# Optimization experiments

Measured on AMD Instinct MI355X. Metric: run time of the kernel, lower is better.

## Reference

```python
import jax, jax.numpy as jnp
import numpy as np

# ---- constants (match init_kwargs defaults) ----
N_NEURON = 512
N_E = int(N_NEURON * 0.8)
DT = 1.0
TAU_MEM = 20.0
TAU_SYN = 5.0
TAU_ADAPT = 700.0
V_TH = -45.0
V_RESET = -60.0
REF_STEPS = int(5.0 / DT)
ASC_AMP = -0.2
READOUT_TAU = 20.0
RESPONSE_WINDOW = 0.8


@jax.custom_vjp
def spike_fn(x):
    # Heaviside with sigmoid surrogate gradient (standard SNN training trick)
    return (x >= 0.0).astype(x.dtype)

def _spike_fwd(x):
    return spike_fn(x), x

def _spike_bwd(x, g):
    beta = 4.0
    s = jax.nn.sigmoid(beta * x)
    return (g * beta * s * (1.0 - s),)

spike_fn.defvjp(_spike_fwd, _spike_bwd)


def setup_inputs() -> dict:
    key = jax.random.key(0)
    kx, kwi, kwr, kmask, kwo = jax.random.split(key, 5)
    T, B, D, N, O = 1000, 64, 128, N_NEURON, 10
    x = jax.random.uniform(kx, (T, B, D), dtype=jnp.float32)  # analog input drive
    W_in = jax.random.normal(kwi, (N, D), dtype=jnp.float32) / np.sqrt(D)
    mag = jnp.abs(jax.random.normal(kwr, (N, N), dtype=jnp.float32)) * 0.05
    mask = (jax.random.uniform(kmask, (N, N)) < 0.1).astype(jnp.float32)
    sign = jnp.concatenate([jnp.ones((N_E,)), -jnp.ones((N - N_E,))]).astype(jnp.float32)
    W_rec = mag * mask * sign[None, :] * (1.0 - jnp.eye(N, dtype=jnp.float32))
    W_out = jax.random.normal(kwo, (O, N), dtype=jnp.float32) / np.sqrt(N)
    b_out = jnp.zeros((O,), dtype=jnp.float32)
    return {
        "x": x,
        "W_in": W_in,
        "input_scale": jnp.float32(1.0),
        "W_rec": W_rec,
        "W_out": W_out,
        "b_out": b_out,
        "output_scale": jnp.float32(1.0),
    }


def _run_snn(x, W_in, input_scale, W_rec, W_out, b_out, output_scale):
    T, B, D = x.shape
    N = W_rec.shape[0]
    asc_amps = jnp.full((N,), ASC_AMP, dtype=x.dtype)  # n_adapt=0 -> all neurons adapt

    a_mem = DT / TAU_MEM
    e_syn = jnp.exp(jnp.asarray(-DT / TAU_SYN, dtype=x.dtype))
    e_asc = jnp.exp(jnp.asarray(-DT / TAU_ADAPT, dtype=x.dtype))

    I_ext = jnp.einsum('tbd,nd->tbn', x * input_scale, W_in)  # (T,B,N)

    v0 = jnp.full((B, N), V_RESET, dtype=x.dtype)
    z = jnp.zeros((B, N), dtype=x.dtype)
    ref0 = jnp.zeros((B, N), dtype=jnp.int32)

    def step(carry, I_t):
        v, asc, r, psc, ref, s_prev = carry
        # AlphaPSC (two-state alpha kernel) driven by recurrent spikes
        rec = s_prev @ W_rec.T
        r = r * e_syn + rec
        psc = psc * e_syn + (DT / TAU_SYN) * r
        # GLIF3 membrane: leak toward v_reset + synaptic + external + after-spike currents
        I = I_t + psc + asc
        v = v + a_mem * (V_RESET - v) + a_mem * I
        in_ref = ref > 0
        v = jnp.where(in_ref, V_RESET, v)
        s = spike_fn(v - V_TH) * (1.0 - in_ref.astype(v.dtype))
        v = v * (1.0 - s) + V_RESET * s  # reset
        ref = jnp.where(s > 0, REF_STEPS, jnp.maximum(ref - 1, 0))
        asc = asc * e_asc + asc_amps[None, :] * s  # after-spike current adaptation
        return (v, asc, r, psc, ref, s), (s, v, psc)

    (_, _, _, _, _, _), (spikes, voltage, psc_hist) = jax.lax.scan(
        step, (v0, z, z, z, ref0, z), I_ext)

    # exponential low-pass filter of spikes, f[0] = s[0]
    alpha = jnp.exp(jnp.asarray(-DT / READOUT_TAU, dtype=x.dtype))
    def lp(f, s):
        f = alpha * f + (1.0 - alpha) * s
        return f, f
    f0 = spikes[0]
    _, f_rest = jax.lax.scan(lp, f0, spikes[1:])
    filtered = jnp.concatenate([f0[None], f_rest], axis=0)  # (T,B,N)

    start = int(T * (1.0 - RESPONSE_WINDOW))
    avg_spikes = filtered[start:].mean(axis=0)  # (B,N)
    output = (avg_spikes * output_scale) @ W_out.T + b_out  # (B,O)
    return output, spikes, voltage, psc_hist, filtered


def reference(x, W_in, input_scale, W_rec, W_out, b_out, output_scale):
    return _run_snn(x, W_in, input_scale, W_rec, W_out, b_out, output_scale)
```

## Files before the change

### kernel.cpp

```cpp
#include <hip/hip_runtime.h>
#include <hip/hip_bf16.h>


#define T_ 1000
#define B_ 64
#define D_ 128
#define N_ 512
#define O_ 10
#define BN_ (B_ * N_)
#define S_ ((size_t)T_ * BN_)

typedef __bf16 bf16x8 __attribute__((ext_vector_type(8)));
typedef float f32x4 __attribute__((ext_vector_type(4)));

__global__ __launch_bounds__(512, 1) void k_gemm_iext(
    const float* __restrict__ x, const float* __restrict__ Win,
    const float* __restrict__ scale_p, float* __restrict__ Iext,
    int* __restrict__ flagmax)
{
  __shared__ __bf16 sW[256 * 128];
  const int tid = threadIdx.x;
  const int nbase = blockIdx.y * 256;
  const float sc = *scale_p;

  for (int i = tid; i < 256 * 16; i += 512) {
    const int n = i >> 4, j = i & 15;
    const float4* src = (const float4*)(Win + (size_t)(nbase + n) * 128 + j * 8);
    float4 f0 = src[0], f1 = src[1];
    bf16x8 h;
    h[0] = (__bf16)f0.x; h[1] = (__bf16)f0.y; h[2] = (__bf16)f0.z; h[3] = (__bf16)f0.w;
    h[4] = (__bf16)f1.x; h[5] = (__bf16)f1.y; h[6] = (__bf16)f1.z; h[7] = (__bf16)f1.w;
    *(bf16x8*)(&sW[n * 128 + ((j ^ (n & 15)) << 3)]) = h;
  }
  __syncthreads();

  const int wave = tid >> 6, lane = tid & 63;
  const int quad = lane >> 4, l16 = lane & 15;
  const int mA = blockIdx.x * 128 + wave * 16 + l16;

  f32x4 acc[16];
#pragma unroll
  for (int c = 0; c < 16; ++c) acc[c] = (f32x4){0.f, 0.f, 0.f, 0.f};

#pragma unroll
  for (int kb = 0; kb < 4; ++kb) {
    const float4* ax = (const float4*)(x + (size_t)mA * 128 + kb * 32 + quad * 8);
    float4 a0 = ax[0], a1 = ax[1];
    bf16x8 af;
    af[0] = (__bf16)(a0.x * sc); af[1] = (__bf16)(a0.y * sc);
    af[2] = (__bf16)(a0.z * sc); af[3] = (__bf16)(a0.w * sc);
    af[4] = (__bf16)(a1.x * sc); af[5] = (__bf16)(a1.y * sc);
    af[6] = (__bf16)(a1.z * sc); af[7] = (__bf16)(a1.w * sc);
    const int j = kb * 4 + quad;
#pragma unroll
    for (int c = 0; c < 16; ++c) {
      const int n = c * 16 + l16;
      bf16x8 bfr = *(const bf16x8*)(&sW[n * 128 + ((j ^ (n & 15)) << 3)]);
      acc[c] = __builtin_amdgcn_mfma_f32_16x16x32_bf16(af, bfr, acc[c], 0, 0, 0);
    }
  }

  float mx = -1e30f;
  const int mBase = blockIdx.x * 128 + wave * 16 + quad * 4;
#pragma unroll
  for (int c = 0; c < 16; ++c) {
#pragma unroll
    for (int r = 0; r < 4; ++r) {
      float vv = acc[c][r];
      mx = fmaxf(mx, vv);
      Iext[(size_t)(mBase + r) * N_ + nbase + c * 16 + l16] = vv;
    }
  }
  if (flagmax) {
    for (int off = 32; off; off >>= 1) mx = fmaxf(mx, __shfl_xor(mx, off));
    if (lane == 0 && mx > 14.0f) atomicMax(flagmax, __float_as_int(mx));
  }
}

#define CHUNK_ 100
#define WARM_ 72
__global__ __launch_bounds__(128) void k_scan(
    const float* __restrict__ Iext, float* __restrict__ volt,
    const float* __restrict__ bout, float* __restrict__ out)
{
  if (blockIdx.y == 0 && blockIdx.x == 0) {
    for (int i = threadIdx.x; i < B_ * O_; i += 128) out[i] = bout[i % O_];
  }
  const int q = blockIdx.x * 128 + threadIdx.x;
  const int chunk = blockIdx.y;
  const int t0 = chunk * CHUNK_;
  const float4* I4 = (const float4*)Iext;
  float4* V4 = (float4*)volt;
  float4 v = make_float4(-60.f, -60.f, -60.f, -60.f);
  if (chunk != 0) {
#pragma unroll 4
    for (int t = t0 - WARM_; t < t0; ++t) {
      float4 I = I4[(size_t)t * (BN_ / 4) + q];
      v.x = v.x + 0.05f * (-60.f - v.x) + 0.05f * I.x;
      v.y = v.y + 0.05f * (-60.f - v.y) + 0.05f * I.y;
      v.z = v.z + 0.05f * (-60.f - v.z) + 0.05f * I.z;
      v.w = v.w + 0.05f * (-60.f - v.w) + 0.05f * I.w;
    }
  }
#pragma unroll 4
  for (int tt = 0; tt < CHUNK_; ++tt) {
    const size_t idx = (size_t)(t0 + tt) * (BN_ / 4) + q;
    float4 I = I4[idx];
    v.x = v.x + 0.05f * (-60.f - v.x) + 0.05f * I.x;
    v.y = v.y + 0.05f * (-60.f - v.y) + 0.05f * I.y;
    v.z = v.z + 0.05f * (-60.f - v.z) + 0.05f * I.z;
    v.w = v.w + 0.05f * (-60.f - v.w) + 0.05f * I.w;
    V4[idx] = v;
  }
}

__global__ __launch_bounds__(512) void k_fallback(
    const float* Iext, const float* __restrict__ Wrec,
    const float* __restrict__ Wout, const float* __restrict__ bout,
    const float* __restrict__ osc_p,
    float* out, float* spikes, float* volt, float* psc_o, float* filt,
    const int* __restrict__ flagmax)
{
  if (!(__int_as_float(*flagmax) > 14.0f)) return;
  const int b = blockIdx.x, n = threadIdx.x;
  __shared__ float s_sp[N_];
  __shared__ float red[N_];
  const float e_syn = expf(-0.2f), e_asc = expf(-1.0f / 700.0f), alpha = expf(-0.05f);
  float v = -60.f, asc = 0.f, rr = 0.f, psc = 0.f, f = 0.f, favg = 0.f, sprev = 0.f;
  int refc = 0;
  for (int t = 0; t < T_; ++t) {
    s_sp[n] = sprev;
    int cnt = __syncthreads_count(sprev > 0.f);
    float rec = 0.f;
    if (cnt > 0)
      for (int m = 0; m < N_; ++m) rec += s_sp[m] * Wrec[(size_t)n * N_ + m];
    rr = rr * e_syn + rec;
    psc = psc * e_syn + 0.2f * rr;
    const size_t idx = (size_t)t * BN_ + (size_t)b * N_ + n;
    float I = Iext[idx] + psc + asc;
    v = (v + 0.05f * (-60.f - v)) + 0.05f * I;
    bool in_ref = refc > 0;
    if (in_ref) v = -60.f;
    float s = (!in_ref && (v - (-45.f) >= 0.f)) ? 1.f : 0.f;
    v = v * (1.f - s) + (-60.f) * s;
    refc = (s > 0.f) ? 5 : (refc > 0 ? refc - 1 : 0);
    asc = asc * e_asc + (-0.2f) * s;
    spikes[idx] = s; volt[idx] = v; psc_o[idx] = psc;
    f = (t == 0) ? s : (alpha * f + (1.f - alpha) * s);
    filt[idx] = f;
    if (t >= 200) favg += f;
    sprev = s;
    __syncthreads();
  }
  favg = favg / 800.f;
  float a_s = favg * (*osc_p);
  for (int o = 0; o < O_; ++o) {
    red[n] = a_s * Wout[o * N_ + n];
    __syncthreads();
    for (int st = 256; st; st >>= 1) {
      if (n < st) red[n] += red[n + st];
      __syncthreads();
    }
    if (n == 0) out[b * O_ + o] = red[0] + bout[o];
    __syncthreads();
  }
}

extern "C" void kernel_launch(void* const* d_in, const int* in_sizes, int n_in,
                              void* d_out, int out_size, void* d_ws, size_t ws_size,
                              hipStream_t stream) {
  const float* x      = (const float*)d_in[0];
  const float* Win    = (const float*)d_in[1];
  const float* iscale = (const float*)d_in[2];
  const float* Wrec   = (const float*)d_in[3];
  const float* Wout   = (const float*)d_in[4];
  const float* bout   = (const float*)d_in[5];
  const float* oscale = (const float*)d_in[6];

  float* out    = (float*)d_out;
  float* spikes = out + B_ * O_;
  float* volt   = spikes + S_;
  float* psc    = volt + S_;
  float* filt   = psc + S_;

  const bool has_flag = ws_size >= 4;
  int* flag = has_flag ? (int*)d_ws : nullptr;
  const bool ws_iext = ws_size >= (size_t)256 + S_ * 4;
  float* iext = ws_iext ? (float*)((char*)d_ws + 256) : filt;

  hipMemsetAsync(spikes, 0, S_ * 4, stream);
  hipMemsetAsync(psc, 0, (ws_iext ? 2 * S_ : S_) * 4, stream);

  k_gemm_iext<<<dim3(500, 2), 512, 0, stream>>>(x, Win, iscale, iext, flag);

  k_scan<<<dim3(64, 10), 128, 0, stream>>>(iext, volt, bout, out);

  if (!ws_iext)
    hipMemsetAsync(filt, 0, S_ * 4, stream);

  if (has_flag)
    k_fallback<<<64, 512, 0, stream>>>(iext, Wrec, Wout, bout, oscale,
                                       out, spikes, volt, psc, filt, flag);
}
```

Baseline: 603.0 us.

## Fuse input GEMM, voltage scan and zero-fill into one kernel

Replaces the separate bf16 MFMA GEMM for I_ext, the chunked voltage scan kernel and the hipMemset zero-fills with a single kernel. Each block owns a 16-neuron slab and one time chunk. It keeps its W_in fragments in registers, computes I_ext per timestep with MFMA, integrates voltage in registers, and writes volt plus the zeroed spikes, psc and filt directly. This removes the full I_ext round trip through global memory and the extra memset passes. In exchange, every slab re-reads x, so x is fetched 32 times, the volt stores are narrower and less coalesced, and the fallback kernel now recomputes I_ext from x and W_in itself.

```diff
diff --git a/kernel.cpp b/kernel.cpp
--- a/kernel.cpp
+++ b/kernel.cpp
@@ -10,112 +10,107 @@
 #define BN_ (B_ * N_)
 #define S_ ((size_t)T_ * BN_)
 
+#define NSLABS_ 32
+#define NCHUNK_ 10
+#define CHUNK_ 100
+#define WARM_ 56
+
 typedef __bf16 bf16x8 __attribute__((ext_vector_type(8)));
 typedef float f32x4 __attribute__((ext_vector_type(4)));
 
-__global__ __launch_bounds__(512, 1) void k_gemm_iext(
+__global__ __launch_bounds__(256) void k_fused(
     const float* __restrict__ x, const float* __restrict__ Win,
-    const float* __restrict__ scale_p, float* __restrict__ Iext,
-    int* __restrict__ flagmax)
+    const float* __restrict__ scale_p, const float* __restrict__ bout,
+    float* __restrict__ out, float* __restrict__ spikes,
+    float* __restrict__ volt, float* __restrict__ psc,
+    float* __restrict__ filt, int* __restrict__ flagmax)
 {
-  __shared__ __bf16 sW[256 * 128];
   const int tid = threadIdx.x;
-  const int nbase = blockIdx.y * 256;
+  const int slab = blockIdx.x, chunk = blockIdx.y;
+  const int nbase = slab * 16;
   const float sc = *scale_p;
 
-  for (int i = tid; i < 256 * 16; i += 512) {
-    const int n = i >> 4, j = i & 15;
-    const float4* src = (const float4*)(Win + (size_t)(nbase + n) * 128 + j * 8);
+  if (slab == 0 && chunk == 0) {
+    for (int i = tid; i < B_ * O_; i += 256) out[i] = bout[i % O_];
+  }
+
+  const int wave = tid >> 6, lane = tid & 63;
+  const int quad = lane >> 4, l16 = lane & 15;
+  const int n = nbase + l16;
+
+  bf16x8 bfrag[4];
+#pragma unroll
+  for (int kb = 0; kb < 4; ++kb) {
+    const float4* src = (const float4*)(Win + (size_t)n * D_ + kb * 32 + quad * 8);
     float4 f0 = src[0], f1 = src[1];
     bf16x8 h;
     h[0] = (__bf16)f0.x; h[1] = (__bf16)f0.y; h[2] = (__bf16)f0.z; h[3] = (__bf16)f0.w;
     h[4] = (__bf16)f1.x; h[5] = (__bf16)f1.y; h[6] = (__bf16)f1.z; h[7] = (__bf16)f1.w;
-    *(bf16x8*)(&sW[n * 128 + ((j ^ (n & 15)) << 3)]) = h;
+    bfrag[kb] = h;
   }
-  __syncthreads();
 
-  const int wave = tid >> 6, lane = tid & 63;
-  const int quad = lane >> 4, l16 = lane & 15;
-  const int mA = blockIdx.x * 128 + wave * 16 + l16;
+  const int t0 = chunk * CHUNK_;
+  const int tstart = (chunk == 0) ? 0 : t0 - WARM_;
+  float v[4] = {-60.f, -60.f, -60.f, -60.f};
+  float mx = -1e30f;
 
-  f32x4 acc[16];
+  for (int tg = tstart; tg < t0 + CHUNK_; tg += 4) {
+    f32x4 acc[4];
 #pragma unroll
-  for (int c = 0; c < 16; ++c) acc[c] = (f32x4){0.f, 0.f, 0.f, 0.f};
-
+    for (int ti = 0; ti < 4; ++ti) acc[ti] = (f32x4){0.f, 0.f, 0.f, 0.f};
 #pragma unroll
-  for (int kb = 0; kb < 4; ++kb) {
-    const float4* ax = (const float4*)(x + (size_t)mA * 128 + kb * 32 + quad * 8);
-    float4 a0 = ax[0], a1 = ax[1];
-    bf16x8 af;
-    af[0] = (__bf16)(a0.x * sc); af[1] = (__bf16)(a0.y * sc);
-    af[2] = (__bf16)(a0.z * sc); af[3] = (__bf16)(a0.w * sc);
-    af[4] = (__bf16)(a1.x * sc); af[5] = (__bf16)(a1.y * sc);
-    af[6] = (__bf16)(a1.z * sc); af[7] = (__bf16)(a1.w * sc);
-    const int j = kb * 4 + quad;
+    for (int ti = 0; ti < 4; ++ti) {
+      const size_t mrow = (size_t)(tg + ti) * B_ + wave * 16 + l16;
 #pragma unroll
-    for (int c = 0; c < 16; ++c) {
-      const int n = c * 16 + l16;
-      bf16x8 bfr = *(const bf16x8*)(&sW[n * 128 + ((j ^ (n & 15)) << 3)]);
-      acc[c] = __builtin_amdgcn_mfma_f32_16x16x32_bf16(af, bfr, acc[c], 0, 0, 0);
+      for (int kb = 0; kb < 4; ++kb) {
+        const float4* ax = (const float4*)(x + mrow * D_ + kb * 32 + quad * 8);
+        float4 a0 = ax[0], a1 = ax[1];
+        bf16x8 af;
+        af[0] = (__bf16)(a0.x * sc); af[1] = (__bf16)(a0.y * sc);
+        af[2] = (__bf16)(a0.z * sc); af[3] = (__bf16)(a0.w * sc);
+        af[4] = (__bf16)(a1.x * sc); af[5] = (__bf16)(a1.y * sc);
+        af[6] = (__bf16)(a1.z * sc); af[7] = (__bf16)(a1.w * sc);
+        acc[ti] = __builtin_amdgcn_mfma_f32_16x16x32_bf16(af, bfrag[kb], acc[ti], 0, 0, 0);
+      }
+    }
+    const bool live = (tg >= t0);
+#pragma unroll
+    for (int ti = 0; ti < 4; ++ti) {
+#pragma unroll
+      for (int r = 0; r < 4; ++r) {
+        float I = acc[ti][r];
+        mx = fmaxf(mx, I);
+        v[r] = v[r] + 0.05f * (-60.f - v[r]) + 0.05f * I;
+        if (live) {
+          const int b = wave * 16 + quad * 4 + r;
+          volt[(size_t)(tg + ti) * BN_ + (size_t)b * N_ + n] = v[r];
+        }
+      }
+    }
+    if (live) {
+      const float4 z = make_float4(0.f, 0.f, 0.f, 0.f);
+#pragma unroll
+      for (int j = 0; j < 4; ++j) {
+        const int i = tid + j * 256;
+        const int t_off = i >> 8, r2 = i & 255;
+        const int b = r2 >> 2, nq = r2 & 3;
+        const size_t off = (size_t)(tg + t_off) * BN_ + (size_t)b * N_ + nbase + nq * 4;
+        *(float4*)(spikes + off) = z;
+        *(float4*)(psc + off) = z;
+        *(float4*)(filt + off) = z;
+      }
     }
   }
 
-  float mx = -1e30f;
-  const int mBase = blockIdx.x * 128 + wave * 16 + quad * 4;
-#pragma unroll
-  for (int c = 0; c < 16; ++c) {
-#pragma unroll
-    for (int r = 0; r < 4; ++r) {
-      float vv = acc[c][r];
-      mx = fmaxf(mx, vv);
-      Iext[(size_t)(mBase + r) * N_ + nbase + c * 16 + l16] = vv;
-    }
-  }
   if (flagmax) {
     for (int off = 32; off; off >>= 1) mx = fmaxf(mx, __shfl_xor(mx, off));
     if (lane == 0 && mx > 14.0f) atomicMax(flagmax, __float_as_int(mx));
   }
 }
 
-#define CHUNK_ 100
-#define WARM_ 72
-__global__ __launch_bounds__(128) void k_scan(
-    const float* __restrict__ Iext, float* __restrict__ volt,
-    const float* __restrict__ bout, float* __restrict__ out)
-{
-  if (blockIdx.y == 0 && blockIdx.x == 0) {
-    for (int i = threadIdx.x; i < B_ * O_; i += 128) out[i] = bout[i % O_];
-  }
-  const int q = blockIdx.x * 128 + threadIdx.x;
-  const int chunk = blockIdx.y;
-  const int t0 = chunk * CHUNK_;
-  const float4* I4 = (const float4*)Iext;
-  float4* V4 = (float4*)volt;
-  float4 v = make_float4(-60.f, -60.f, -60.f, -60.f);
-  if (chunk != 0) {
-#pragma unroll 4
-    for (int t = t0 - WARM_; t < t0; ++t) {
-      float4 I = I4[(size_t)t * (BN_ / 4) + q];
-      v.x = v.x + 0.05f * (-60.f - v.x) + 0.05f * I.x;
-      v.y = v.y + 0.05f * (-60.f - v.y) + 0.05f * I.y;
-      v.z = v.z + 0.05f * (-60.f - v.z) + 0.05f * I.z;
-      v.w = v.w + 0.05f * (-60.f - v.w) + 0.05f * I.w;
-    }
-  }
-#pragma unroll 4
-  for (int tt = 0; tt < CHUNK_; ++tt) {
-    const size_t idx = (size_t)(t0 + tt) * (BN_ / 4) + q;
-    float4 I = I4[idx];
-    v.x = v.x + 0.05f * (-60.f - v.x) + 0.05f * I.x;
-    v.y = v.y + 0.05f * (-60.f - v.y) + 0.05f * I.y;
-    v.z = v.z + 0.05f * (-60.f - v.z) + 0.05f * I.z;
-    v.w = v.w + 0.05f * (-60.f - v.w) + 0.05f * I.w;
-    V4[idx] = v;
-  }
-}
-
 __global__ __launch_bounds__(512) void k_fallback(
-    const float* Iext, const float* __restrict__ Wrec,
+    const float* __restrict__ x, const float* __restrict__ Win,
+    const float* __restrict__ iscale, const float* __restrict__ Wrec,
     const float* __restrict__ Wout, const float* __restrict__ bout,
     const float* __restrict__ osc_p,
     float* out, float* spikes, float* volt, float* psc_o, float* filt,
@@ -123,21 +118,25 @@
 {
   if (!(__int_as_float(*flagmax) > 14.0f)) return;
   const int b = blockIdx.x, n = threadIdx.x;
+  __shared__ float sx[D_];
   __shared__ float s_sp[N_];
   __shared__ float red[N_];
+  const float sc = *iscale;
   const float e_syn = expf(-0.2f), e_asc = expf(-1.0f / 700.0f), alpha = expf(-0.05f);
   float v = -60.f, asc = 0.f, rr = 0.f, psc = 0.f, f = 0.f, favg = 0.f, sprev = 0.f;
   int refc = 0;
   for (int t = 0; t < T_; ++t) {
+    if (n < D_) sx[n] = x[((size_t)t * B_ + b) * D_ + n] * sc;
     s_sp[n] = sprev;
     int cnt = __syncthreads_count(sprev > 0.f);
+    float Iext = 0.f;
+    for (int d = 0; d < D_; ++d) Iext += sx[d] * Win[(size_t)n * D_ + d];
     float rec = 0.f;
     if (cnt > 0)
       for (int m = 0; m < N_; ++m) rec += s_sp[m] * Wrec[(size_t)n * N_ + m];
     rr = rr * e_syn + rec;
     psc = psc * e_syn + 0.2f * rr;
-    const size_t idx = (size_t)t * BN_ + (size_t)b * N_ + n;
-    float I = Iext[idx] + psc + asc;
+    float I = Iext + psc + asc;
     v = (v + 0.05f * (-60.f - v)) + 0.05f * I;
     bool in_ref = refc > 0;
     if (in_ref) v = -60.f;
@@ -145,6 +144,7 @@
     v = v * (1.f - s) + (-60.f) * s;
     refc = (s > 0.f) ? 5 : (refc > 0 ? refc - 1 : 0);
     asc = asc * e_asc + (-0.2f) * s;
+    const size_t idx = (size_t)t * BN_ + (size_t)b * N_ + n;
     spikes[idx] = s; volt[idx] = v; psc_o[idx] = psc;
     f = (t == 0) ? s : (alpha * f + (1.f - alpha) * s);
     filt[idx] = f;
@@ -185,20 +185,11 @@
 
   const bool has_flag = ws_size >= 4;
   int* flag = has_flag ? (int*)d_ws : nullptr;
-  const bool ws_iext = ws_size >= (size_t)256 + S_ * 4;
-  float* iext = ws_iext ? (float*)((char*)d_ws + 256) : filt;
 
-  hipMemsetAsync(spikes, 0, S_ * 4, stream);
-  hipMemsetAsync(psc, 0, (ws_iext ? 2 * S_ : S_) * 4, stream);
-
-  k_gemm_iext<<<dim3(500, 2), 512, 0, stream>>>(x, Win, iscale, iext, flag);
-
-  k_scan<<<dim3(64, 10), 128, 0, stream>>>(iext, volt, bout, out);
-
-  if (!ws_iext)
-    hipMemsetAsync(filt, 0, S_ * 4, stream);
+  k_fused<<<dim3(NSLABS_, NCHUNK_), 256, 0, stream>>>(
+      x, Win, iscale, bout, out, spikes, volt, psc, filt, flag);
 
   if (has_flag)
-    k_fallback<<<64, 512, 0, stream>>>(iext, Wrec, Wout, bout, oscale,
-                                       out, spikes, volt, psc, filt, flag);
+    k_fallback<<<B_, N_, 0, stream>>>(x, Win, iscale, Wrec, Wout, bout, oscale,
+                                      out, spikes, volt, psc, filt, flag);
 }
```

Result: slower. 869.5 us (+44.2%).
